# Kernel optimization log

Hardware: AMD Instinct MI355X
Metric: run time of the kernel (lower is better)

Reference implementation:

```python
import jax, jax.numpy as jnp
import numpy as np

N, E, G, H = 5000, 50000, 8, 4
GAT_DIMS = [(1536, 1024), (1024, 512), (512, 256)]
MLP_DIMS = [(256, 128), (128, 64), (64, 32), (32, 16), (16, 1)]
GATE_DIMS = [(256, 128), (128, 1)]
NEG_SLOPE = 0.2
EPS = 1e-16


def setup_inputs() -> dict:
    key = jax.random.key(0)
    keys = iter(jax.random.split(key, 80))

    def nrm(shape, s=0.05):
        return jax.random.normal(next(keys), shape, jnp.float32) * s

    inp = {}
    inp["x"] = jax.random.normal(next(keys), (N, 1536), jnp.float32)
    inp["edge_index"] = jax.random.randint(next(keys), (2, E), 0, N)
    inp["batch"] = jnp.sort(jax.random.randint(next(keys), (N,), 0, G))
    for i, (di, do) in enumerate(GAT_DIMS, 1):
        inp[f"Wl{i}"] = nrm((di, H * do))
        inp[f"bl{i}"] = jnp.zeros((H * do,), jnp.float32)
        inp[f"Wr{i}"] = nrm((di, H * do))
        inp[f"br{i}"] = jnp.zeros((H * do,), jnp.float32)
        inp[f"att{i}"] = nrm((H, do))
        inp[f"b{i}"] = jnp.zeros((do,), jnp.float32)
    for i, (di, do) in enumerate(MLP_DIMS):
        inp[f"Wm{i}"] = nrm((di, do))
        inp[f"bm{i}"] = jnp.zeros((do,), jnp.float32)
    for i, (di, do) in enumerate(GATE_DIMS):
        inp[f"Wg{i}"] = nrm((di, do))
        inp[f"bg{i}"] = jnp.zeros((do,), jnp.float32)
    return inp


def _gatv2(x, src, dst, Wl, bl, Wr, br, att, bias):
    # PyG GATv2Conv, concat=False: mean over heads.
    C = att.shape[1]
    xl = (x @ Wl + bl).reshape(-1, H, C)  # source-side transform [N,H,C]
    xr = (x @ Wr + br).reshape(-1, H, C)  # target-side transform [N,H,C]
    # edge scores: att . leaky_relu(x_j + x_i)  -> [E',H]
    s = jnp.sum(jax.nn.leaky_relu(xl[src] + xr[dst], negative_slope=NEG_SLOPE) * att, axis=-1)
    # segment softmax over destination node neighborhoods
    m = jax.ops.segment_max(s, dst, num_segments=N)
    ex = jnp.exp(s - m[dst])
    den = jax.ops.segment_sum(ex, dst, num_segments=N)
    alpha = ex / (den[dst] + EPS)
    out = jax.ops.segment_sum(alpha[:, :, None] * xl[src], dst, num_segments=N)  # [N,H,C]
    return out.mean(axis=1) + bias


def _forward(x, edge_index, batch, params):
    loop = jnp.arange(N)
    src = jnp.concatenate([edge_index[0], loop])  # add_self_loops=True (PyG default)
    dst = jnp.concatenate([edge_index[1], loop])
    for i in (1, 2, 3):
        x = jax.nn.relu(_gatv2(x, src, dst,
                               params[f"Wl{i}"], params[f"bl{i}"],
                               params[f"Wr{i}"], params[f"br{i}"],
                               params[f"att{i}"], params[f"b{i}"]))
    # AttentionalAggregation: segment-softmax(gate_nn(x)) weighted sum over graphs
    gate = jax.nn.relu(x @ params["Wg0"] + params["bg0"]) @ params["Wg1"] + params["bg1"]
    g = gate[:, 0]
    m = jax.ops.segment_max(g, batch, num_segments=G)
    ex = jnp.exp(g - m[batch])
    den = jax.ops.segment_sum(ex, batch, num_segments=G)
    w = ex / (den[batch] + EPS)
    h = jax.ops.segment_sum(w[:, None] * x, batch, num_segments=G)  # [G,256]
    for i in range(4):
        h = jax.nn.relu(h @ params[f"Wm{i}"] + params[f"bm{i}"])
    return h @ params["Wm4"] + params["bm4"]  # [G,1]


def reference(x, edge_index, batch,
              Wl1, bl1, Wr1, br1, att1, b1,
              Wl2, bl2, Wr2, br2, att2, b2,
              Wl3, bl3, Wr3, br3, att3, b3,
              Wm0, bm0, Wm1, bm1, Wm2, bm2, Wm3, bm3, Wm4, bm4,
              Wg0, bg0, Wg1, bg1):
    params = dict(locals())
    for k in ("x", "edge_index", "batch"):
        params.pop(k)
    return _forward(x, edge_index, batch, params)
```

## Files before the change

kernel.cpp:

```cpp
#include <hip/hip_runtime.h>
#include <math.h>
#include <type_traits>

#define NN 5000
#define NNP 5120
#define NE 50000
#define NEE 55000
#define NG 8
#define NH 4

typedef __attribute__((ext_vector_type(8))) _Float16 half8;
typedef __attribute__((ext_vector_type(4))) _Float16 half4;
typedef __attribute__((ext_vector_type(4))) float floatx4;


__device__ inline float waveSum(float v) {
    #pragma unroll
    for (int o = 32; o > 0; o >>= 1) v += __shfl_xor(v, o, 64);
    return v;
}
__device__ inline float waveMax(float v) {
    #pragma unroll
    for (int o = 32; o > 0; o >>= 1) v = fmaxf(v, __shfl_xor(v, o, 64));
    return v;
}

__device__ __forceinline__ void gload_lds16(const _Float16* g, _Float16* l) {
    __builtin_amdgcn_global_load_lds(
        (__attribute__((address_space(1))) void*)g,
        (__attribute__((address_space(3))) void*)l,
        16, 0, 0);
}

template<int N>
__device__ __forceinline__ void vmgate() {
    if constexpr (N == 0) asm volatile("s_waitcnt vmcnt(0)" ::: "memory");
    else if constexpr (N == 2) asm volatile("s_waitcnt vmcnt(2)" ::: "memory");
    else if constexpr (N == 4) asm volatile("s_waitcnt vmcnt(4)" ::: "memory");
}


__global__ void k_cvtA(const float* __restrict__ X, _Float16* __restrict__ A0, int n) {
    int i = blockIdx.x * 256 + threadIdx.x;
    if (i >= n) return;
    A0[i] = (_Float16)X[i];
}

__global__ __launch_bounds__(256) void k_cvtWT(const float* __restrict__ W,
        _Float16* __restrict__ B0, int K, int M)
{
    __shared__ float tile[32][33];
    int m0 = blockIdx.x * 32, k0 = blockIdx.y * 32;
    int tx = threadIdx.x & 31, ty = threadIdx.x >> 5;
    #pragma unroll
    for (int i = 0; i < 4; ++i)
        tile[ty + 8 * i][tx] = W[(size_t)(k0 + ty + 8 * i) * M + m0 + tx];
    __syncthreads();
    #pragma unroll
    for (int i = 0; i < 4; ++i) {
        int mm = ty + 8 * i, kk = tx;
        B0[(size_t)(m0 + mm) * K + kk + k0] = (_Float16)tile[kk][mm];
    }
}

__global__ __launch_bounds__(512, 2) void gemm256_mfma_f16(
    const _Float16* __restrict__ A0, const _Float16* __restrict__ B0,
    const float* __restrict__ biasL, const float* __restrict__ biasR,
    int Nhalf, _Float16* __restrict__ C,
    int Mrows, int K, int N)
{
    __shared__ __align__(16) _Float16 smem[2 * 32768];

    const int tid  = threadIdx.x;
    const int wave = tid >> 6;
    const int lane = tid & 63;
    const int wr = wave >> 2;
    const int wc = wave & 3;
    const int rowBase = blockIdx.y * 256;
    const int colBase = blockIdx.x * 256;

    floatx4 acc[2][2][4][2];
    #pragma unroll
    for (int qa = 0; qa < 2; ++qa)
        #pragma unroll
        for (int qb = 0; qb < 2; ++qb)
            #pragma unroll
            for (int f = 0; f < 4; ++f)
                #pragma unroll
                for (int g = 0; g < 2; ++g)
                    acc[qa][qb][f][g] = (floatx4){0.f, 0.f, 0.f, 0.f};

    const int srow   = lane >> 3;
    const int schunk = ((lane & 7) ^ srow) << 3;
    const _Float16* gA = A0 + (size_t)(rowBase + wave * 16 + srow) * K + schunk;
    const _Float16* gB = B0 + (size_t)(colBase + wave * 16 + srow) * K + schunk;
    const size_t rstep = (size_t)8 * K;
    const size_t hstep = (size_t)128 * K;

    auto stageA = [&](int b, int h, int kt) {
        _Float16* l = &smem[b * 32768 + (h * 128 + wave * 16) * 64];
        const _Float16* g = gA + (size_t)h * hstep + (size_t)kt * 64;
        gload_lds16(g, l);
        gload_lds16(g + rstep, l + 512);
    };
    auto stageB = [&](int b, int h, int kt) {
        _Float16* l = &smem[b * 32768 + 16384 + (h * 128 + wave * 16) * 64];
        const _Float16* g = gB + (size_t)h * hstep + (size_t)kt * 64;
        gload_lds16(g, l);
        gload_lds16(g + rstep, l + 512);
    };

    const int lm  = lane & 15;
    const int key = lane & 7;
    const int kg  = lane >> 4;

    half8 af[4][2];
    half8 bf0[2][2];
    half8 bf1[2][2];

    auto readA = [&](const _Float16* Ab, int QA) {
        #pragma unroll
        for (int f = 0; f < 4; ++f)
            #pragma unroll
            for (int s = 0; s < 2; ++s) {
                int row = QA * 128 + wr * 64 + f * 16 + lm;
                int ch = (s * 4 + kg) ^ key;
                af[f][s] = *(const half8*)&Ab[row * 64 + ch * 8];
            }
    };
    auto readB = [&](const _Float16* Bb, int QB, half8 (&bf)[2][2]) {
        #pragma unroll
        for (int g = 0; g < 2; ++g)
            #pragma unroll
            for (int s = 0; s < 2; ++s) {
                int row = QB * 128 + wc * 32 + g * 16 + lm;
                int ch = (s * 4 + kg) ^ key;
                bf[g][s] = *(const half8*)&Bb[row * 64 + ch * 8];
            }
    };
    constexpr std::integral_constant<int, 0> I0{};
    constexpr std::integral_constant<int, 1> I1{};
    auto mfma16 = [&](auto QAc, auto QBc, half8 (&bf)[2][2]) {
        constexpr int QA = decltype(QAc)::value;
        constexpr int QB = decltype(QBc)::value;
        __builtin_amdgcn_s_setprio(1);
        #pragma unroll
        for (int f = 0; f < 4; ++f)
            #pragma unroll
            for (int g = 0; g < 2; ++g)
                #pragma unroll
                for (int s = 0; s < 2; ++s)
                    acc[QA][QB][f][g] = __builtin_amdgcn_mfma_f32_16x16x32_f16(
                        af[f][s], bf[g][s], acc[QA][QB][f][g], 0, 0, 0);
        __builtin_amdgcn_s_setprio(0);
    };

    stageA(0, 0, 0); stageB(0, 0, 0); stageB(0, 1, 0); stageA(0, 1, 0);
    vmgate<4>();
    __builtin_amdgcn_s_barrier();

    const int nk = K >> 6;
    for (int t = 0; t < nk - 1; ++t) {
        const int b = t & 1;
        const _Float16* Ab = &smem[b * 32768];
        const _Float16* Bb = Ab + 16384;
        readA(Ab, 0); readB(Bb, 0, bf0);
        stageA(b ^ 1, 0, t + 1);
        __builtin_amdgcn_s_barrier();
        mfma16(I0, I0, bf0);
        vmgate<4>();
        __builtin_amdgcn_s_barrier();
        __builtin_amdgcn_sched_barrier(0);
        readB(Bb, 1, bf1);
        stageB(b ^ 1, 0, t + 1);
        __builtin_amdgcn_s_barrier();
        mfma16(I0, I1, bf1);
        vmgate<4>();
        __builtin_amdgcn_s_barrier();
        __builtin_amdgcn_sched_barrier(0);
        readA(Ab, 1);
        stageB(b ^ 1, 1, t + 1);
        __builtin_amdgcn_s_barrier();
        mfma16(I1, I0, bf0);
        __builtin_amdgcn_s_barrier();
        __builtin_amdgcn_sched_barrier(0);
        stageA(b ^ 1, 1, t + 1);
        __builtin_amdgcn_s_barrier();
        mfma16(I1, I1, bf1);
        vmgate<4>();
        __builtin_amdgcn_s_barrier();
        __builtin_amdgcn_sched_barrier(0);
    }
    {
        const int b = (nk - 1) & 1;
        const _Float16* Ab = &smem[b * 32768];
        const _Float16* Bb = Ab + 16384;
        readA(Ab, 0); readB(Bb, 0, bf0);
        __builtin_amdgcn_s_barrier();
        mfma16(I0, I0, bf0);
        vmgate<2>();
        __builtin_amdgcn_s_barrier();
        readB(Bb, 1, bf1);
        __builtin_amdgcn_s_barrier();
        mfma16(I0, I1, bf1);
        vmgate<0>();
        __builtin_amdgcn_s_barrier();
        readA(Ab, 1);
        __builtin_amdgcn_s_barrier();
        mfma16(I1, I0, bf0);
        __builtin_amdgcn_s_barrier();
        mfma16(I1, I1, bf1);
        __builtin_amdgcn_s_barrier();
    }

    _Float16* Ct = smem;
    const int cq = (lane >> 4) * 4;
    #pragma unroll
    for (int qb = 0; qb < 2; ++qb)
        #pragma unroll
        for (int g = 0; g < 2; ++g) {
            int col = qb * 128 + wc * 32 + g * 16 + lm;
            int gcol = colBase + col;
            float bv = (gcol < Nhalf) ? biasL[gcol] : biasR[gcol - Nhalf];
            #pragma unroll
            for (int qa = 0; qa < 2; ++qa)
                #pragma unroll
                for (int f = 0; f < 4; ++f)
                    #pragma unroll
                    for (int r = 0; r < 4; ++r) {
                        int row = qa * 128 + wr * 64 + f * 16 + cq + r;
                        int gi = (col >> 4) ^ ((row >> 2) & 7);
                        Ct[row * 256 + gi * 16 + (col & 15)] =
                            (_Float16)(acc[qa][qb][f][g][r] + bv);
                    }
        }
    __syncthreads();
    const int r0 = tid >> 5;
    const int cc = (tid & 31) * 8;
    const int gg = cc >> 4;
    #pragma unroll
    for (int ps = 0; ps < 16; ++ps) {
        int row = ps * 16 + r0;
        int grow = rowBase + row;
        if (grow < Mrows) {
            int gp = gg ^ ((row >> 2) & 7);
            half8 v = *(const half8*)&Ct[row * 256 + gp * 16 + (cc & 15)];
            *(half8*)&C[(size_t)grow * N + colBase + cc] = v;
        }
    }
}

__global__ __launch_bounds__(256) void gemm_mfma_f16(
    const _Float16* __restrict__ A0, const _Float16* __restrict__ B0,
    const float* __restrict__ biasL, const float* __restrict__ biasR,
    int Nhalf, _Float16* __restrict__ C,
    int Mrows, int K, int N)
{
    __shared__ __align__(16) _Float16 smem[2 * 2 * 128 * 32];
    _Float16* As = smem;
    _Float16* Bs = smem + 2 * 128 * 32;

    const int tid = threadIdx.x;
    const int wave = tid >> 6;
    const int lane = tid & 63;
    const int wm = (wave >> 1) * 64;
    const int wn = (wave & 1) * 64;
    const int lm = lane & 15;
    const int swz = (((lane >> 4) ^ ((lane >> 1) & 3)) << 3);

    const int rowBase = blockIdx.y * 128;
    const int colBase = blockIdx.x * 128;

    floatx4 acc[4][4];
    #pragma unroll
    for (int i = 0; i < 4; ++i)
        #pragma unroll
        for (int j = 0; j < 4; ++j)
            acc[i][j] = (floatx4){0.f, 0.f, 0.f, 0.f};

    const int sr = lane >> 2;
    const int scol = (((lane & 3) ^ ((lane >> 3) & 3)) << 3);
    const _Float16* gA = A0 + (size_t)(rowBase + wave * 32 + sr) * K + scol;
    const _Float16* gB = B0 + (size_t)(colBase + wave * 32 + sr) * K + scol;
    const size_t skip16 = (size_t)16 * K;
    const int lo0 = (wave * 32) * 32;
    const int lo1 = (wave * 32 + 16) * 32;

    gload_lds16(gA, &As[lo0]);
    gload_lds16(gA + skip16, &As[lo1]);
    gload_lds16(gB, &Bs[lo0]);
    gload_lds16(gB + skip16, &Bs[lo1]);
    __syncthreads();

    const int nk = K >> 5;
    for (int t = 0; t < nk; ++t) {
        const int p = t & 1;
        const int po = p * 128 * 32;
        if (t + 1 < nk) {
            const int k1 = (t + 1) << 5;
            const int qo = (p ^ 1) * 128 * 32;
            gload_lds16(gA + k1, &As[qo + lo0]);
            gload_lds16(gA + skip16 + k1, &As[qo + lo1]);
            gload_lds16(gB + k1, &Bs[qo + lo0]);
            gload_lds16(gB + skip16 + k1, &Bs[qo + lo1]);
        }
        half8 a0[4], b0[4];
        #pragma unroll
        for (int i = 0; i < 4; ++i) {
            a0[i] = *(const half8*)&As[po + (wm + i * 16 + lm) * 32 + swz];
            b0[i] = *(const half8*)&Bs[po + (wn + i * 16 + lm) * 32 + swz];
        }
        #pragma unroll
        for (int i = 0; i < 4; ++i)
            #pragma unroll
            for (int j = 0; j < 4; ++j)
                acc[i][j] = __builtin_amdgcn_mfma_f32_16x16x32_f16(a0[i], b0[j], acc[i][j], 0, 0, 0);
        __syncthreads();
    }

    _Float16* Ct = smem;
    const int cq = (lane >> 4) * 4;
    #pragma unroll
    for (int j = 0; j < 4; ++j) {
        int col = wn + j * 16 + lm;
        int gcol = colBase + col;
        float bv = (gcol < Nhalf) ? biasL[gcol] : biasR[gcol - Nhalf];
        #pragma unroll
        for (int i = 0; i < 4; ++i) {
            int row = wm + i * 16 + cq;
            #pragma unroll
            for (int r = 0; r < 4; ++r) {
                int rr = row + r;
                Ct[rr * 128 + (col ^ (((rr >> 2) & 7) << 4))] = (_Float16)(acc[i][j][r] + bv);
            }
        }
    }
    __syncthreads();
    const int r0 = tid >> 4;
    const int cc = (tid & 15) * 8;
    #pragma unroll
    for (int ps = 0; ps < 8; ++ps) {
        int row = ps * 16 + r0;
        int grow = rowBase + row;
        if (grow < Mrows) {
            half8 v = *(const half8*)&Ct[row * 128 + (cc ^ (((row >> 2) & 7) << 4))];
            *(half8*)&C[(size_t)grow * N + colBase + cc] = v;
        }
    }
}


__global__ void k_build_edges(const int* __restrict__ ei, int* __restrict__ src,
                              int* __restrict__ dst) {
    int i = blockIdx.x * 256 + threadIdx.x;
    if (i < NE) { src[i] = ei[i]; dst[i] = ei[NE + i]; }
    else if (i < NEE) { src[i] = i - NE; dst[i] = i - NE; }
}

__global__ void k_zero32(unsigned int* __restrict__ p, int n) {
    int i = blockIdx.x * 256 + threadIdx.x;
    if (i < n) p[i] = 0u;
}

__global__ void k_count(const int* __restrict__ dst, int* __restrict__ cnt) {
    int i = blockIdx.x * 256 + threadIdx.x;
    if (i < NEE) atomicAdd(&cnt[dst[i]], 1);
}

__global__ __launch_bounds__(256) void k_scan(const int* __restrict__ cnt,
                                              int* __restrict__ off, int* __restrict__ cur) {
    __shared__ int partial[256];
    __shared__ int ppre[257];
    int t = threadIdx.x;
    const int chunk = (NN + 255) / 256;
    int lo = t * chunk, hi = min(NN, (t + 1) * chunk);
    int s = 0;
    for (int i = lo; i < hi; ++i) s += cnt[i];
    partial[t] = s;
    __syncthreads();
    if (t == 0) {
        int acc = 0;
        for (int i = 0; i < 256; ++i) { ppre[i] = acc; acc += partial[i]; }
        ppre[256] = acc;
    }
    __syncthreads();
    int acc = ppre[t];
    for (int i = lo; i < hi; ++i) { off[i] = acc; cur[i] = acc; acc += cnt[i]; }
    if (t == 0) off[NN] = ppre[256];
}

__global__ void k_fill(const int* __restrict__ src, const int* __restrict__ dst,
                       int* __restrict__ cur, int* __restrict__ slist) {
    int e = blockIdx.x * 256 + threadIdx.x;
    if (e < NEE) { int p = atomicAdd(&cur[dst[e]], 1); slist[p] = src[e]; }
}

template<int C>
__global__ __launch_bounds__(256) void k_gat_fused(
    const _Float16* __restrict__ xlr, const float* __restrict__ att,
    const int* __restrict__ eoff, const int* __restrict__ slist,
    const float* __restrict__ bias, _Float16* __restrict__ out)
{
    constexpr int LD = 2 * NH * C;
    constexpr int CH = (C >= 512) ? 8 : 4;
    constexpr int NC = C / (64 * CH);
    constexpr int PL = NC * CH;
    __shared__ float red[NH * C];
    const int n = blockIdx.x;
    const int h = threadIdx.x >> 6;
    const int lane = threadIdx.x & 63;

    float xrv[PL], attv[PL], acc[PL];
    {
        const _Float16* xrrow = xlr + (size_t)n * LD + NH * C + h * C + lane * CH;
        const float* ah = att + h * C + lane * CH;
        #pragma unroll
        for (int c = 0; c < NC; ++c) {
            if constexpr (CH == 8) {
                half8 hv = *(const half8*)(xrrow + c * 64 * CH);
                #pragma unroll
                for (int e = 0; e < 8; ++e) xrv[c * 8 + e] = (float)hv[e];
            } else {
                half4 hv = *(const half4*)(xrrow + c * 64 * CH);
                #pragma unroll
                for (int e = 0; e < 4; ++e) xrv[c * 4 + e] = (float)hv[e];
            }
            #pragma unroll
            for (int e = 0; e < CH; e += 4) {
                float4 a4 = *(const float4*)(ah + c * 64 * CH + e);
                attv[c * CH + e + 0] = a4.x; attv[c * CH + e + 1] = a4.y;
                attv[c * CH + e + 2] = a4.z; attv[c * CH + e + 3] = a4.w;
            }
        }
        #pragma unroll
        for (int e = 0; e < PL; ++e) acc[e] = 0.f;
    }

    float m = -INFINITY, den = 0.f;
    const int start = eoff[n], end = eoff[n + 1];

    _Float16 bufA[PL], bufB[PL];
    auto ldrow = [&](int s, _Float16* buf) {
        const _Float16* p = xlr + (size_t)s * LD + h * C + lane * CH;
        #pragma unroll
        for (int c = 0; c < NC; ++c) {
            if constexpr (CH == 8)
                *(half8*)&buf[c * 8] = *(const half8*)(p + c * 64 * CH);
            else
                *(half4*)&buf[c * 4] = *(const half4*)(p + c * 64 * CH);
        }
    };

    if (start < end) ldrow(slist[start], bufA);
    for (int j = start; j < end; ++j) {
        if (j + 1 < end) ldrow(slist[j + 1], bufB);
        float xv[PL];
        float ps = 0.f;
        #pragma unroll
        for (int e = 0; e < PL; ++e) {
            xv[e] = (float)bufA[e];
            float v = xv[e] + xrv[e];
            v = v > 0.f ? v : 0.2f * v;
            ps = fmaf(v, attv[e], ps);
        }
        ps = waveSum(ps);
        float m_new = fmaxf(m, ps);
        float scale = expf(m - m_new);
        float ex = expf(ps - m_new);
        den = den * scale + ex;
        m = m_new;
        #pragma unroll
        for (int e = 0; e < PL; ++e)
            acc[e] = fmaf(ex, xv[e], acc[e] * scale);
        #pragma unroll
        for (int e = 0; e < PL; ++e) bufA[e] = bufB[e];
    }

    float inv = 1.f / (den + 1e-16f);
    #pragma unroll
    for (int c = 0; c < NC; ++c) {
        int off = h * C + c * 64 * CH + lane * CH;
        #pragma unroll
        for (int e = 0; e < CH; e += 4) {
            float4 r;
            r.x = acc[c * CH + e + 0] * inv;
            r.y = acc[c * CH + e + 1] * inv;
            r.z = acc[c * CH + e + 2] * inv;
            r.w = acc[c * CH + e + 3] * inv;
            *(float4*)&red[off + e] = r;
        }
    }
    __syncthreads();

    int t = threadIdx.x;
    for (int c4 = t; c4 < C / 4; c4 += 256) {
        int c = c4 * 4;
        float4 r0 = *(const float4*)&red[0 * C + c];
        float4 r1 = *(const float4*)&red[1 * C + c];
        float4 r2 = *(const float4*)&red[2 * C + c];
        float4 r3 = *(const float4*)&red[3 * C + c];
        float4 bv = *(const float4*)(bias + c);
        half4 o;
        o[0] = (_Float16)fmaxf((r0.x + r1.x + r2.x + r3.x) * 0.25f + bv.x, 0.f);
        o[1] = (_Float16)fmaxf((r0.y + r1.y + r2.y + r3.y) * 0.25f + bv.y, 0.f);
        o[2] = (_Float16)fmaxf((r0.z + r1.z + r2.z + r3.z) * 0.25f + bv.z, 0.f);
        o[3] = (_Float16)fmaxf((r0.w + r1.w + r2.w + r3.w) * 0.25f + bv.w, 0.f);
        *(half4*)(out + (size_t)n * C + c) = o;
    }
}


__global__ __launch_bounds__(128) void k_gate(
    const _Float16* __restrict__ x, const float* __restrict__ Wg0,
    const float* __restrict__ bg0, const float* __restrict__ Wg1,
    const float* __restrict__ bg1, float* __restrict__ g)
{
    int n = blockIdx.x;
    int t = threadIdx.x;
    __shared__ float xs[256];
    __shared__ float wsum[2];
    const _Float16* xp = x + (size_t)n * 256;
    xs[t] = (float)xp[t]; xs[t + 128] = (float)xp[t + 128];
    __syncthreads();
    float acc = bg0[t];
    for (int k = 0; k < 256; ++k) acc = fmaf(xs[k], Wg0[k * 128 + t], acc);
    acc = acc > 0.f ? acc : 0.f;
    float prod = acc * Wg1[t];
    prod = waveSum(prod);
    if ((t & 63) == 0) wsum[t >> 6] = prod;
    __syncthreads();
    if (t == 0) g[n] = wsum[0] + wsum[1] + bg1[0];
}

__global__ void k_group_bounds(const int* __restrict__ batch, int* __restrict__ gstart,
                               int* __restrict__ gend) {
    int n = blockIdx.x * 256 + threadIdx.x;
    if (n >= NN) return;
    int b = batch[n];
    if (n == 0 || batch[n - 1] != b) gstart[b] = n;
    if (n == NN - 1 || batch[n + 1] != b) gend[b] = n + 1;
}

__global__ __launch_bounds__(256) void k_pool_stats(
    const float* __restrict__ g, const int* __restrict__ gstart,
    const int* __restrict__ gend, float* __restrict__ mOut,
    float* __restrict__ invdenOut)
{
    int gi = blockIdx.x;
    int t = threadIdx.x;
    int s0 = gstart[gi], e0 = gend[gi];
    __shared__ float red[4];
    float mx = -1e30f;
    for (int n = s0 + t; n < e0; n += 256) mx = fmaxf(mx, g[n]);
    float wm = waveMax(mx);
    if ((t & 63) == 0) red[t >> 6] = wm;
    __syncthreads();
    float m = fmaxf(fmaxf(red[0], red[1]), fmaxf(red[2], red[3]));
    __syncthreads();
    float sm = 0.f;
    for (int n = s0 + t; n < e0; n += 256) sm += expf(g[n] - m);
    sm = waveSum(sm);
    if ((t & 63) == 0) red[t >> 6] = sm;
    __syncthreads();
    if (t == 0) {
        float den = red[0] + red[1] + red[2] + red[3] + 1e-16f;
        mOut[gi] = m;
        invdenOut[gi] = 1.f / den;
    }
}

#define PCH 16
__global__ __launch_bounds__(256) void k_pool_acc(
    const _Float16* __restrict__ x, const float* __restrict__ g,
    const int* __restrict__ batch, const float* __restrict__ m,
    const float* __restrict__ invden, float* __restrict__ hpool)
{
    int base = blockIdx.x * PCH;
    int t = threadIdx.x;
    float acc = 0.f;
    int cur = -1;
    for (int i = 0; i < PCH; ++i) {
        int n = base + i;
        if (n >= NN) break;
        int b = batch[n];
        if (b != cur) {
            if (cur >= 0) atomicAdd(&hpool[cur * 256 + t], acc);
            cur = b; acc = 0.f;
        }
        float w = expf(g[n] - m[b]) * invden[b];
        acc = fmaf(w, (float)x[(size_t)n * 256 + t], acc);
    }
    if (cur >= 0) atomicAdd(&hpool[cur * 256 + t], acc);
}

__global__ __launch_bounds__(256) void k_mlp(
    const float* __restrict__ hpool,
    const float* __restrict__ Wm0, const float* __restrict__ bm0,
    const float* __restrict__ Wm1, const float* __restrict__ bm1,
    const float* __restrict__ Wm2, const float* __restrict__ bm2,
    const float* __restrict__ Wm3, const float* __restrict__ bm3,
    const float* __restrict__ Wm4, const float* __restrict__ bm4,
    float* __restrict__ out)
{
    __shared__ float bufA[8 * 256];
    __shared__ float bufB[8 * 128];
    int t = threadIdx.x;
    for (int i = t; i < 8 * 256; i += 256) bufA[i] = hpool[i];
    __syncthreads();
    for (int i = t; i < 8 * 128; i += 256) {
        int r = i >> 7, c = i & 127;
        float acc = bm0[c];
        for (int k = 0; k < 256; ++k) acc = fmaf(bufA[r * 256 + k], Wm0[k * 128 + c], acc);
        bufB[i] = fmaxf(acc, 0.f);
    }
    __syncthreads();
    for (int i = t; i < 8 * 64; i += 256) {
        int r = i >> 6, c = i & 63;
        float acc = bm1[c];
        for (int k = 0; k < 128; ++k) acc = fmaf(bufB[r * 128 + k], Wm1[k * 64 + c], acc);
        bufA[i] = fmaxf(acc, 0.f);
    }
    __syncthreads();
    for (int i = t; i < 8 * 32; i += 256) {
        int r = i >> 5, c = i & 31;
        float acc = bm2[c];
        for (int k = 0; k < 64; ++k) acc = fmaf(bufA[r * 64 + k], Wm2[k * 32 + c], acc);
        bufB[i] = fmaxf(acc, 0.f);
    }
    __syncthreads();
    for (int i = t; i < 8 * 16; i += 256) {
        int r = i >> 4, c = i & 15;
        float acc = bm3[c];
        for (int k = 0; k < 32; ++k) acc = fmaf(bufB[r * 32 + k], Wm3[k * 16 + c], acc);
        bufA[i] = fmaxf(acc, 0.f);
    }
    __syncthreads();
    if (t < 8) {
        float acc = bm4[0];
        for (int k = 0; k < 16; ++k) acc = fmaf(bufA[t * 16 + k], Wm4[k], acc);
        out[t] = acc;
    }
}


static void run_gat_layer(const _Float16* ain, int K, int C,
                          const float* Wl, const float* bl,
                          const float* Wr, const float* br,
                          const float* att, const float* bias,
                          _Float16* wb0, _Float16* xlr,
                          const int* eoff, const int* slist,
                          _Float16* xout, hipStream_t stream)
{
    int HC = NH * C;
    dim3 tgrid(HC / 32, K / 32);
    k_cvtWT<<<tgrid, 256, 0, stream>>>(Wl, wb0, K, HC);
    k_cvtWT<<<tgrid, 256, 0, stream>>>(Wr, wb0 + (size_t)HC * K, K, HC);
    if (C >= 512) {
        dim3 ggrid(2 * HC / 256, NNP / 256);
        gemm256_mfma_f16<<<ggrid, 512, 0, stream>>>(ain, wb0, bl, br, HC, xlr, NN, K, 2 * HC);
    } else {
        dim3 ggrid(2 * HC / 128, NNP / 128);
        gemm_mfma_f16<<<ggrid, 256, 0, stream>>>(ain, wb0, bl, br, HC, xlr, NN, K, 2 * HC);
    }

    if (C == 1024)
        k_gat_fused<1024><<<NN, 256, 0, stream>>>(xlr, att, eoff, slist, bias, xout);
    else if (C == 512)
        k_gat_fused<512><<<NN, 256, 0, stream>>>(xlr, att, eoff, slist, bias, xout);
    else
        k_gat_fused<256><<<NN, 256, 0, stream>>>(xlr, att, eoff, slist, bias, xout);
}

extern "C" void kernel_launch(void* const* d_in, const int* in_sizes, int n_in,
                              void* d_out, int out_size, void* d_ws, size_t ws_size,
                              hipStream_t stream) {
    const float* x      = (const float*)d_in[0];
    const int* ei       = (const int*)d_in[1];
    const int* batch    = (const int*)d_in[2];
    const float* Wl1 = (const float*)d_in[3];  const float* bl1 = (const float*)d_in[4];
    const float* Wr1 = (const float*)d_in[5];  const float* br1 = (const float*)d_in[6];
    const float* att1= (const float*)d_in[7];  const float* b1  = (const float*)d_in[8];
    const float* Wl2 = (const float*)d_in[9];  const float* bl2 = (const float*)d_in[10];
    const float* Wr2 = (const float*)d_in[11]; const float* br2 = (const float*)d_in[12];
    const float* att2= (const float*)d_in[13]; const float* b2  = (const float*)d_in[14];
    const float* Wl3 = (const float*)d_in[15]; const float* bl3 = (const float*)d_in[16];
    const float* Wr3 = (const float*)d_in[17]; const float* br3 = (const float*)d_in[18];
    const float* att3= (const float*)d_in[19]; const float* b3  = (const float*)d_in[20];
    const float* Wm0 = (const float*)d_in[21]; const float* bm0 = (const float*)d_in[22];
    const float* Wm1 = (const float*)d_in[23]; const float* bm1 = (const float*)d_in[24];
    const float* Wm2 = (const float*)d_in[25]; const float* bm2 = (const float*)d_in[26];
    const float* Wm3 = (const float*)d_in[27]; const float* bm3 = (const float*)d_in[28];
    const float* Wm4 = (const float*)d_in[29]; const float* bm4 = (const float*)d_in[30];
    const float* Wg0 = (const float*)d_in[31]; const float* bg0 = (const float*)d_in[32];
    const float* Wg1 = (const float*)d_in[33]; const float* bg1 = (const float*)d_in[34];
    float* out = (float*)d_out;

    float* ws = (float*)d_ws;
    size_t o = 0;
    _Float16* xlr = (_Float16*)(ws + o); o += (size_t)NNP * 8192 / 2;
    _Float16* x1  = (_Float16*)(ws + o); o += (size_t)NNP * 1024 / 2;
    _Float16* x2  = (_Float16*)(ws + o); o += (size_t)NNP * 512 / 2;
    _Float16* x3  = (_Float16*)(ws + o); o += (size_t)NNP * 256 / 2;
    _Float16* a0p = (_Float16*)(ws + o); o += (size_t)NNP * 1536 / 2;
    _Float16* wb0 = (_Float16*)(ws + o); o += (size_t)8192 * 1536 / 2;
    int* srcA    = (int*)(ws + o); o += NEE;
    int* dstA    = (int*)(ws + o); o += NEE;
    int* cnt     = (int*)(ws + o); o += NN;
    int* eoff    = (int*)(ws + o); o += NN + 1;
    int* cur     = (int*)(ws + o); o += NN;
    int* slist   = (int*)(ws + o); o += NEE;
    float* g     = ws + o; o += NN;
    int* gstart  = (int*)(ws + o); o += NG;
    int* gend    = (int*)(ws + o); o += NG;
    float* gm    = ws + o; o += NG;
    float* ginv  = ws + o; o += NG;
    float* hpool = ws + o; o += NG * 256;

    int ebB = (NEE + 255) / 256;
    k_build_edges<<<ebB, 256, 0, stream>>>(ei, srcA, dstA);
    k_zero32<<<(NN + 255) / 256, 256, 0, stream>>>((unsigned int*)cnt, NN);
    k_count<<<ebB, 256, 0, stream>>>(dstA, cnt);
    k_scan<<<1, 256, 0, stream>>>(cnt, eoff, cur);
    k_fill<<<ebB, 256, 0, stream>>>(srcA, dstA, cur, slist);

    int nA = NN * 1536;
    k_cvtA<<<(nA + 255) / 256, 256, 0, stream>>>(x, a0p, nA);

    run_gat_layer(a0p, 1536, 1024, Wl1, bl1, Wr1, br1, att1, b1,
                  wb0, xlr, eoff, slist, x1, stream);
    run_gat_layer(x1,  1024, 512,  Wl2, bl2, Wr2, br2, att2, b2,
                  wb0, xlr, eoff, slist, x2, stream);
    run_gat_layer(x2,  512,  256,  Wl3, bl3, Wr3, br3, att3, b3,
                  wb0, xlr, eoff, slist, x3, stream);

    k_gate<<<NN, 128, 0, stream>>>(x3, Wg0, bg0, Wg1, bg1, g);
    k_zero32<<<1, 64, 0, stream>>>((unsigned int*)gstart, 2 * NG);
    k_group_bounds<<<(NN + 255) / 256, 256, 0, stream>>>(batch, gstart, gend);
    k_pool_stats<<<NG, 256, 0, stream>>>(g, gstart, gend, gm, ginv);
    k_zero32<<<(NG * 256 + 255) / 256, 256, 0, stream>>>((unsigned int*)hpool, NG * 256);
    k_pool_acc<<<(NN + PCH - 1) / PCH, 256, 0, stream>>>(x3, g, batch, gm, ginv, hpool);
    k_mlp<<<1, 256, 0, stream>>>(hpool, Wm0, bm0, Wm1, bm1, Wm2, bm2,
                                 Wm3, bm3, Wm4, bm4, out);
}
```

Before: 668.2 us.

## Double-buffer A fragments and prefetch next tile's A during last MFMA

Splits the A register fragments into two buffers so the next k-tile's first A quadrant is read from LDS while the final MFMA block of the current tile runs. An extra vmgate is added before that prefetch so the staged data is resident, and the sched_barrier fences are dropped to give the compiler freedom. This hides LDS read latency at the tile boundary, at the cost of more VGPRs and a riskier schedule.

Result: no change. 672.8 us (+0.7%).

```diff
diff --git a/kernel.cpp b/kernel.cpp
--- a/kernel.cpp
+++ b/kernel.cpp
@@ -1,6 +1,5 @@
 #include <hip/hip_runtime.h>
 #include <math.h>
-#include <type_traits>
 
 #define NN 5000
 #define NNP 5120
@@ -114,11 +113,12 @@
     const int key = lane & 7;
     const int kg  = lane >> 4;
 
-    half8 af[4][2];
+    half8 af0[4][2];
+    half8 af1[4][2];
     half8 bf0[2][2];
     half8 bf1[2][2];
 
-    auto readA = [&](const _Float16* Ab, int QA) {
+    auto readA = [&](const _Float16* Ab, int QA, half8 (&af)[4][2]) {
         #pragma unroll
         for (int f = 0; f < 4; ++f)
             #pragma unroll
@@ -138,11 +138,7 @@
                 bf[g][s] = *(const half8*)&Bb[row * 64 + ch * 8];
             }
     };
-    constexpr std::integral_constant<int, 0> I0{};
-    constexpr std::integral_constant<int, 1> I1{};
-    auto mfma16 = [&](auto QAc, auto QBc, half8 (&bf)[2][2]) {
-        constexpr int QA = decltype(QAc)::value;
-        constexpr int QB = decltype(QBc)::value;
+    auto mfma16 = [&](half8 (&af)[4][2], half8 (&bf)[2][2], floatx4 (&ac)[4][2]) {
         __builtin_amdgcn_s_setprio(1);
         #pragma unroll
         for (int f = 0; f < 4; ++f)
@@ -150,66 +146,66 @@
             for (int g = 0; g < 2; ++g)
                 #pragma unroll
                 for (int s = 0; s < 2; ++s)
-                    acc[QA][QB][f][g] = __builtin_amdgcn_mfma_f32_16x16x32_f16(
-                        af[f][s], bf[g][s], acc[QA][QB][f][g], 0, 0, 0);
+                    ac[f][g] = __builtin_amdgcn_mfma_f32_16x16x32_f16(
+                        af[f][s], bf[g][s], ac[f][g], 0, 0, 0);
         __builtin_amdgcn_s_setprio(0);
     };
 
     stageA(0, 0, 0); stageB(0, 0, 0); stageB(0, 1, 0); stageA(0, 1, 0);
     vmgate<4>();
     __builtin_amdgcn_s_barrier();
+    readA(&smem[0], 0, af0);
 
     const int nk = K >> 6;
     for (int t = 0; t < nk - 1; ++t) {
         const int b = t & 1;
-        const _Float16* Ab = &smem[b * 32768];
-        const _Float16* Bb = Ab + 16384;
-        readA(Ab, 0); readB(Bb, 0, bf0);
+        const _Float16* Ab  = &smem[b * 32768];
+        const _Float16* Bb  = Ab + 16384;
+        const _Float16* AbN = &smem[(b ^ 1) * 32768];
+        readB(Bb, 0, bf0);
         stageA(b ^ 1, 0, t + 1);
         __builtin_amdgcn_s_barrier();
-        mfma16(I0, I0, bf0);
+        mfma16(af0, bf0, acc[0][0]);
         vmgate<4>();
         __builtin_amdgcn_s_barrier();
-        __builtin_amdgcn_sched_barrier(0);
         readB(Bb, 1, bf1);
         stageB(b ^ 1, 0, t + 1);
         __builtin_amdgcn_s_barrier();
-        mfma16(I0, I1, bf1);
+        mfma16(af0, bf1, acc[0][1]);
         vmgate<4>();
         __builtin_amdgcn_s_barrier();
-        __builtin_amdgcn_sched_barrier(0);
-        readA(Ab, 1);
+        readA(Ab, 1, af1);
         stageB(b ^ 1, 1, t + 1);
         __builtin_amdgcn_s_barrier();
-        mfma16(I1, I0, bf0);
-        __builtin_amdgcn_s_barrier();
-        __builtin_amdgcn_sched_barrier(0);
+        mfma16(af1, bf0, acc[1][0]);
+        vmgate<4>();
+        __builtin_amdgcn_s_barrier();
+        readA(AbN, 0, af0);
         stageA(b ^ 1, 1, t + 1);
         __builtin_amdgcn_s_barrier();
-        mfma16(I1, I1, bf1);
+        mfma16(af1, bf1, acc[1][1]);
         vmgate<4>();
         __builtin_amdgcn_s_barrier();
-        __builtin_amdgcn_sched_barrier(0);
     }
     {
         const int b = (nk - 1) & 1;
         const _Float16* Ab = &smem[b * 32768];
         const _Float16* Bb = Ab + 16384;
-        readA(Ab, 0); readB(Bb, 0, bf0);
-        __builtin_amdgcn_s_barrier();
-        mfma16(I0, I0, bf0);
+        readB(Bb, 0, bf0);
+        __builtin_amdgcn_s_barrier();
+        mfma16(af0, bf0, acc[0][0]);
         vmgate<2>();
         __builtin_amdgcn_s_barrier();
         readB(Bb, 1, bf1);
         __builtin_amdgcn_s_barrier();
-        mfma16(I0, I1, bf1);
+        mfma16(af0, bf1, acc[0][1]);
         vmgate<0>();
         __builtin_amdgcn_s_barrier();
-        readA(Ab, 1);
-        __builtin_amdgcn_s_barrier();
-        mfma16(I1, I0, bf0);
-        __builtin_amdgcn_s_barrier();
-        mfma16(I1, I1, bf1);
+        readA(Ab, 1, af1);
+        __builtin_amdgcn_s_barrier();
+        mfma16(af1, bf0, acc[1][0]);
+        __builtin_amdgcn_s_barrier();
+        mfma16(af1, bf1, acc[1][1]);
         __builtin_amdgcn_s_barrier();
     }
 
```
